# Performance work log

Hardware: AMD Instinct MI355X
Metric: run time of the kernel (lower is better)

## Reference

```python
import jax, jax.numpy as jnp
import numpy as np

B, T, E = 2, 2048, 2048
H, KV, D = 16, 4, 128
N_REP = H // KV
WINDOW = 512
BASE_THETA = 10000.0
MIN_VAL = -1e9


def _rope_cos_sin(seq_len, dim, dtype):
    inv_freq = 1.0 / (BASE_THETA ** (jnp.arange(0, dim, 2, dtype=jnp.float32) / dim))
    ang = jnp.arange(seq_len, dtype=jnp.float32)[:, None] * inv_freq[None, :]  # [T, D/2]
    return jnp.cos(ang).astype(dtype), jnp.sin(ang).astype(dtype)


def _apply_rope(x, cos, sin):
    # x: [B, T, h, D]; rotate-half convention
    x1, x2 = jnp.split(x, 2, axis=-1)
    c = cos[None, :, None, :]
    s = sin[None, :, None, :]
    return jnp.concatenate([x1 * c - x2 * s, x2 * c + x1 * s], axis=-1)


def setup_inputs() -> dict:
    key = jax.random.key(0)
    k1, k2, k3, k4, k5 = jax.random.split(key, 5)
    std = 0.02 / np.sqrt(2 * 24)
    return {
        "x": jax.random.normal(k1, (B, T, E), dtype=jnp.float32),
        "Wq": jax.random.normal(k2, (H * D, E), dtype=jnp.float32) * std,
        "Wk": jax.random.normal(k3, (KV * D, E), dtype=jnp.float32) * std,
        "Wv": jax.random.normal(k4, (KV * D, E), dtype=jnp.float32) * std,
        "Wo": jax.random.normal(k5, (E, E), dtype=jnp.float32) * std,
    }


def reference(x, Wq, Wk, Wv, Wo):
    b, t, e = x.shape
    scale = 1.0 / jnp.sqrt(jnp.float32(D))

    q = (x @ Wq.T).reshape(b, t, H, D)
    k = (x @ Wk.T).reshape(b, t, KV, D)
    v = (x @ Wv.T).reshape(b, t, KV, D)

    cos, sin = _rope_cos_sin(t, D, x.dtype)
    q = _apply_rope(q, cos, sin)
    k = _apply_rope(k, cos, sin)

    # GQA: repeat kv heads to match query heads
    k = jnp.repeat(k, N_REP, axis=2)  # [B, T, H, D]
    v = jnp.repeat(v, N_REP, axis=2)

    scores = jnp.einsum("bqhd,bkhd->bhqk", q, k) * scale  # [B, H, T, T]

    # sliding-window causal additive mask (offset=0)
    rows = jnp.arange(t)[:, None]
    cols = jnp.arange(t)[None, :]
    valid = (cols <= rows) & ((rows - cols) < WINDOW)
    mask = jnp.where(valid, 0.0, MIN_VAL).astype(x.dtype)  # [T, T]
    scores = scores + mask[None, None, :, :]

    attn = jax.nn.softmax(scores, axis=-1)
    out = jnp.einsum("bhqk,bkhd->bqhd", attn, v).reshape(b, t, H * D)
    return out @ Wo.T
```

## Files before the change

kernel.cpp:

```cpp
#include <hip/hip_runtime.h>
#include <hip/hip_bf16.h>
#include <cstdint>

#define TSEQ 2048
#define NB   2
#define NH   16
#define NKV  4
#define HD   128
#define EMB  2048
#define WIN  512

typedef unsigned short u16;
typedef __attribute__((ext_vector_type(8))) short s16x8;
typedef __attribute__((ext_vector_type(4))) float f32x4;
typedef __attribute__((ext_vector_type(16))) float f32x16;
typedef __attribute__((ext_vector_type(4))) unsigned short u16x4;
typedef __attribute__((ext_vector_type(8))) unsigned short u16x8;

__device__ __forceinline__ u16 f2bf(float x) {
    unsigned u = __builtin_bit_cast(unsigned, x);
    u += 0x7fffu + ((u >> 16) & 1u);
    return (u16)(u >> 16);
}
__device__ __forceinline__ float bf2f(u16 u) {
    return __builtin_bit_cast(float, ((unsigned)u) << 16);
}
__device__ __forceinline__ float ex2(float x) {
    return __builtin_amdgcn_exp2f(x);
}

__device__ __forceinline__ void gld_lds16(const void* g, void* l) {
    __builtin_amdgcn_global_load_lds(
        (__attribute__((address_space(1))) void*)(void*)(g),
        (__attribute__((address_space(3))) void*)(l),
        16, 0, 0);
}

__device__ __forceinline__ f32x4 mfma16(s16x8 a, s16x8 b, f32x4 c) {
    return __builtin_amdgcn_mfma_f32_16x16x32_bf16(a, b, c, 0, 0, 0);
}
__device__ __forceinline__ f32x16 mfma32(s16x8 a, s16x8 b, f32x16 c) {
    return __builtin_amdgcn_mfma_f32_32x32x16_bf16(a, b, c, 0, 0, 0);
}

template <int CTRL>
__device__ __forceinline__ float dpp_movf(float x) {
    return __builtin_bit_cast(float,
        __builtin_amdgcn_update_dpp(0, __builtin_bit_cast(int, x), CTRL, 0xF, 0xF, true));
}
__device__ __forceinline__ float dpp_max16(float x) {
    x = fmaxf(x, dpp_movf<0xB1>(x));
    x = fmaxf(x, dpp_movf<0x4E>(x));
    x = fmaxf(x, dpp_movf<0x128>(x));
    x = fmaxf(x, dpp_movf<0x124>(x));
    return x;
}
__device__ __forceinline__ float dpp_sum16(float x) {
    x += dpp_movf<0xB1>(x);
    x += dpp_movf<0x4E>(x);
    x += dpp_movf<0x128>(x);
    x += dpp_movf<0x124>(x);
    return x;
}

__global__ void cast_all(const float* __restrict__ x,  const float* __restrict__ wq,
                         const float* __restrict__ wk, const float* __restrict__ wv,
                         const float* __restrict__ wo,
                         u16* __restrict__ xb, u16* __restrict__ wqb,
                         u16* __restrict__ wkvb, u16* __restrict__ wob,
                         float* __restrict__ tab) {
    if (blockIdx.x >= 18432) {
        int i = (blockIdx.x - 18432) * 256 + threadIdx.x;
        int t = i >> 6, d = i & 63;
        float inv = __expf(-(float)d * (9.210340371976184f / 64.0f));
        float s, c;
        sincosf((float)t * inv, &s, &c);
        tab[i] = c;
        tab[131072 + i] = s;
        return;
    }
    long i = ((long)blockIdx.x * 256 + threadIdx.x) * 4;
    const float* s; u16* d; long off;
    if (i < 8388608L)        { s = x;  d = xb;             off = i; }
    else if (i < 12582912L)  { s = wq; d = wqb;            off = i - 8388608L; }
    else if (i < 13631488L)  { s = wk; d = wkvb;           off = i - 12582912L; }
    else if (i < 14680064L)  { s = wv; d = wkvb + 1048576; off = i - 13631488L; }
    else                     { s = wo; d = wob;            off = i - 14680064L; }
    float4 v = *(const float4*)(s + off);
    u16x4 o;
    o[0] = f2bf(v.x); o[1] = f2bf(v.y); o[2] = f2bf(v.z); o[3] = f2bf(v.w);
    *(u16x4*)(d + off) = o;
}

#define RDFRAG(base, offb, sg, ks) \
    (*(const s16x8*)((base) + (offb) + ((((half) + 2 * (ks)) ^ (sg)) << 4)))

template <int MODE>
__global__ __launch_bounds__(512) void gemm8(const u16* __restrict__ A, const u16* __restrict__ B,
                                             void* __restrict__ Cp, u16* __restrict__ vtp,
                                             u16* __restrict__ kp) {
    constexpr int BN     = (MODE == 3) ? 192 : 128;
    constexpr int NBB    = BN / 64;
    constexpr int K      = 2048;
    constexpr int NTK    = K / 64;
    constexpr int ABYTES = 32768;
    constexpr int BBYTES = BN * 128;
    constexpr int BUFB   = ABYTES + BBYTES;
    constexpr int NLD    = 4 + NBB;

    __shared__ __align__(16) char smem[2 * BUFB];

    const int tid  = threadIdx.x;
    const int lane = tid & 63;
    const int w    = tid >> 6;
    const int l31  = lane & 31;
    const int half = lane >> 5;
    const int wr   = w >> 1;
    const int wc   = w & 1;
    const int bx   = blockIdx.x, by = blockIdx.y;

    const int srow   = w * 8 + (lane >> 3);
    const int schunk = lane & 7;
    const int sdoff  = w * 8 * 128;

    const u16* agp[4];
    const u16* bgp[NBB];
#pragma unroll
    for (int s = 0; s < 4; s++) {
        const int row = s * 64 + srow;
        const int sg  = ((row >> 1) ^ (row >> 2)) & 7;
        agp[s] = A + (size_t)(by * 256 + row) * K + ((schunk ^ sg) << 3);
    }
#pragma unroll
    for (int s = 0; s < NBB; s++) {
        const int row = s * 64 + srow;
        const int sg  = ((row >> 1) ^ (row >> 2)) & 7;
        bgp[s] = B + (size_t)(bx * BN + row) * K + ((schunk ^ sg) << 3);
    }

    int aoffb[2], asg[2];
#pragma unroll
    for (int mi = 0; mi < 2; mi++) {
        const int r = wr * 64 + mi * 32 + l31;
        aoffb[mi] = r * 128;
        asg[mi]   = ((r >> 1) ^ (r >> 2)) & 7;
    }
    int boffb[NBB], bsg[NBB];
#pragma unroll
    for (int nj = 0; nj < NBB; nj++) {
        const int r = wc * (BN / 2) + nj * 32 + l31;
        boffb[nj] = r * 128;
        bsg[nj]   = ((r >> 1) ^ (r >> 2)) & 7;
    }

    f32x16 acc[2][NBB];
#pragma unroll
    for (int mi = 0; mi < 2; mi++)
#pragma unroll
        for (int nj = 0; nj < NBB; nj++)
#pragma unroll
            for (int r = 0; r < 16; r++)
                acc[mi][nj][r] = 0.f;

    auto stage_A = [&](char* base) {
#pragma unroll
        for (int s = 0; s < 4; s++) {
            gld_lds16(agp[s], base + s * 8192 + sdoff);
            agp[s] += 64;
        }
    };
    auto stage_B = [&](char* base) {
#pragma unroll
        for (int s = 0; s < NBB; s++) {
            gld_lds16(bgp[s], base + ABYTES + s * 8192 + sdoff);
            bgp[s] += 64;
        }
    };

    stage_A(smem);        stage_B(smem);
    stage_A(smem + BUFB); stage_B(smem + BUFB);

    for (int t = 0; t < NTK; ++t) {
        char* buf = smem + (t & 1) * BUFB;
        const char* Ab = buf;
        const char* Bb = buf + ABYTES;
        if (t < NTK - 1) asm volatile("s_waitcnt vmcnt(%0)" :: "n"(NLD) : "memory");
        else             asm volatile("s_waitcnt vmcnt(0)" ::: "memory");
        __builtin_amdgcn_s_barrier();

        s16x8 a0[4], a1[4];
        {
            s16x8 bf[4];
#pragma unroll
            for (int ks = 0; ks < 4; ks++) {
                a0[ks] = RDFRAG(Ab, aoffb[0], asg[0], ks);
                a1[ks] = RDFRAG(Ab, aoffb[1], asg[1], ks);
                bf[ks] = RDFRAG(Bb, boffb[0], bsg[0], ks);
            }
            __builtin_amdgcn_s_barrier();
            __builtin_amdgcn_s_setprio(1);
#pragma unroll
            for (int ks = 0; ks < 4; ks++) {
                acc[0][0] = mfma32(a0[ks], bf[ks], acc[0][0]);
                acc[1][0] = mfma32(a1[ks], bf[ks], acc[1][0]);
            }
            __builtin_amdgcn_s_setprio(0);
            __builtin_amdgcn_s_barrier();
        }
        asm volatile("" ::: "memory");
        if (t + 2 < NTK) stage_A(buf);
#pragma unroll
        for (int j = 1; j < NBB; j++) {
            s16x8 bf[4];
#pragma unroll
            for (int ks = 0; ks < 4; ks++)
                bf[ks] = RDFRAG(Bb, boffb[j], bsg[j], ks);
            __builtin_amdgcn_s_barrier();
            __builtin_amdgcn_s_setprio(1);
#pragma unroll
            for (int ks = 0; ks < 4; ks++) {
                acc[0][j] = mfma32(a0[ks], bf[ks], acc[0][j]);
                acc[1][j] = mfma32(a1[ks], bf[ks], acc[1][j]);
            }
            __builtin_amdgcn_s_setprio(0);
            __builtin_amdgcn_s_barrier();
        }
        asm volatile("" ::: "memory");
        if (t + 2 < NTK) stage_B(buf);
    }

    const int row0 = by * 256 + wr * 64;
    if constexpr (MODE == 0) {
        const int col0 = bx * 128 + wc * 64 + l31;
#pragma unroll
        for (int mi = 0; mi < 2; mi++)
#pragma unroll
            for (int nj = 0; nj < 2; nj++)
#pragma unroll
                for (int r = 0; r < 16; r++) {
                    const int crow = row0 + mi * 32 + (r & 3) + 8 * (r >> 2) + 4 * half;
                    ((float*)Cp)[(size_t)crow * 2048 + col0 + nj * 32] = acc[mi][nj][r];
                }
    } else {
#pragma unroll
        for (int nj = 0; nj < NBB; nj++) {
            const int colbase = bx * 192 + wc * 96 + nj * 32;
            if (colbase >= 2560) continue;
            if (colbase < 2048) {
#pragma unroll
                for (int mi = 0; mi < 2; mi++)
#pragma unroll
                    for (int r = 0; r < 16; r++) {
                        const int crow = row0 + mi * 32 + (r & 3) + 8 * (r >> 2) + 4 * half;
                        ((u16*)Cp)[(size_t)crow * 2048 + colbase + l31] = f2bf(acc[mi][nj][r]);
                    }
            } else {
#pragma unroll
                for (int mi = 0; mi < 2; mi++)
#pragma unroll
                    for (int r = 0; r < 16; r++) {
                        const int crow = row0 + mi * 32 + (r & 3) + 8 * (r >> 2) + 4 * half;
                        kp[(size_t)crow * 512 + colbase - 2048 + l31] = f2bf(acc[mi][nj][r]);
                    }
            }
        }
        const int bb = (by * 256) >> 11;
        const int t0 = (by * 256) & (TSEQ - 1);
        u16* tr = (u16*)smem;
#pragma unroll
        for (int wcx = 0; wcx < 2; wcx++)
#pragma unroll
            for (int njx = 0; njx < NBB; njx++) {
                const int colbase = bx * 192 + wcx * 96 + njx * 32;
                if (colbase < 2560) continue;
                __syncthreads();
                if (wc == wcx) {
#pragma unroll
                    for (int mi = 0; mi < 2; mi++)
#pragma unroll
                        for (int r = 0; r < 16; r++) {
                            const int tl = wr * 64 + mi * 32 + (r & 3) + 8 * (r >> 2) + 4 * half;
                            tr[l31 * 264 + tl] = f2bf(acc[mi][njx][r]);
                        }
                }
                __syncthreads();
                const int voff = colbase - 2560;
#pragma unroll
                for (int s = 0; s < 2; s++) {
                    const int slot = s * 512 + tid;
                    const int dl   = slot >> 5;
                    const int tseg = slot & 31;
                    u16x8 val = *(const u16x8*)(tr + dl * 264 + tseg * 8);
                    const int dg = voff + dl;
                    *(u16x8*)(vtp + ((size_t)((bb * NKV + (dg >> 7)) * HD + (dg & 127))) * TSEQ +
                              t0 + tseg * 8) = val;
                }
            }
    }
}

__global__ void rope_k(u16* __restrict__ buf, const float* __restrict__ tab) {
    int i = blockIdx.x * 256 + threadIdx.x;
    int d   = i & 63;
    int hh  = (i >> 6) & 3;
    int row = i >> 8;
    int t   = row & (TSEQ - 1);
    size_t base = (size_t)row * 512 + hh * HD + d;
    float x1 = bf2f(buf[base]);
    float x2 = bf2f(buf[base + 64]);
    float c = tab[t * 64 + d];
    float s = tab[131072 + t * 64 + d];
    buf[base]      = f2bf(x1 * c - x2 * s);
    buf[base + 64] = f2bf(x2 * c + x1 * s);
}

__global__ __launch_bounds__(256, 3) void attn_kernel(const u16* __restrict__ qb, const u16* __restrict__ kb,
                                                      const u16* __restrict__ vt, const float* __restrict__ tab,
                                                      u16* __restrict__ ao) {
    __shared__ __align__(16) char smem[40960];
    u16* ks = (u16*)smem;
    u16* vs = (u16*)(smem + 16384);
    u16* Pl = (u16*)(smem + 32768);

    const int tid  = threadIdx.x;
    const int w    = tid >> 6;
    const int lane = tid & 63;
    const int l15  = lane & 15;
    const int quad = lane >> 4;
    const int id   = blockIdx.x;
    const int kv   = id & 3;
    const int b    = (id >> 2) & 1;
    const int q0   = (id >> 3) * 16;
    const int h    = kv * 4 + w;
    u16* Pw = Pl + w * 1024;
    const float scale2 = 0.1275174089593282f;

    const u16* kbase = kb + (size_t)b * TSEQ * 512 + kv * HD;
    const u16* vbase = vt + (size_t)(b * NKV + kv) * HD * TSEQ;

    s16x8 aq[4];
    {
        const u16* qrow = qb + (size_t)(b * TSEQ + q0 + l15) * EMB + h * HD + quad * 8;
        const float* ct = tab + (size_t)(q0 + l15) * 64 + quad * 8;
        float qf[4][8], cs[2][8], sn[2][8];
        *(float4*)(&cs[0][0]) = *(const float4*)(ct);
        *(float4*)(&cs[0][4]) = *(const float4*)(ct + 4);
        *(float4*)(&cs[1][0]) = *(const float4*)(ct + 32);
        *(float4*)(&cs[1][4]) = *(const float4*)(ct + 36);
        *(float4*)(&sn[0][0]) = *(const float4*)(ct + 131072);
        *(float4*)(&sn[0][4]) = *(const float4*)(ct + 131076);
        *(float4*)(&sn[1][0]) = *(const float4*)(ct + 131104);
        *(float4*)(&sn[1][4]) = *(const float4*)(ct + 131108);
#pragma unroll
        for (int c = 0; c < 4; c++)
#pragma unroll
            for (int e = 0; e < 8; e++)
                qf[c][e] = bf2f(qrow[c * 32 + e]);
#pragma unroll
        for (int c = 0; c < 2; c++)
#pragma unroll
            for (int e = 0; e < 8; e++) {
                float x1 = qf[c][e], x2 = qf[c + 2][e];
                qf[c][e]     = x1 * cs[c][e] - x2 * sn[c][e];
                qf[c + 2][e] = x2 * cs[c][e] + x1 * sn[c][e];
            }
#pragma unroll
        for (int c = 0; c < 4; c++)
#pragma unroll
            for (int e = 0; e < 8; e++)
                aq[c][e] = (short)f2bf(qf[c][e]);
    }

    f32x4 o[8];
#pragma unroll
    for (int n = 0; n < 8; n++) o[n] = f32x4{0.f, 0.f, 0.f, 0.f};
    float mrow[4] = {-1e30f, -1e30f, -1e30f, -1e30f};
    float lrow[4] = {0.f, 0.f, 0.f, 0.f};

    int kb0 = q0 - (WIN - 1);
    if (kb0 < 0) kb0 = 0;
    kb0 &= ~63;

    for (int kbi = kb0; kbi <= q0 + 15; kbi += 64) {
#pragma unroll
        for (int s = 0; s < 4; s++) {
            int slot = s * 256 + tid;
            int i    = slot >> 4;
            int lc   = (slot & 15) ^ (i & 7);
            gld_lds16(kbase + (size_t)(kbi + i) * 512 + lc * 8, (char*)ks + slot * 16);
        }
#pragma unroll
        for (int s = 0; s < 4; s++) {
            int slot = s * 256 + tid;
            int d    = slot >> 3;
            int lc   = (slot & 7) ^ (d & 7);
            gld_lds16(vbase + (size_t)d * TSEQ + kbi + lc * 8, (char*)vs + slot * 16);
        }
        __syncthreads();

        f32x4 sv[4];
#pragma unroll
        for (int kt = 0; kt < 4; kt++) sv[kt] = f32x4{0.f, 0.f, 0.f, 0.f};
#pragma unroll
        for (int c = 0; c < 4; c++) {
            s16x8 bk[4];
#pragma unroll
            for (int kt = 0; kt < 4; kt++) {
                int sc = (c * 4 + quad) ^ (l15 & 7);
                bk[kt] = *(const s16x8*)(ks + (kt * 16 + l15) * 128 + sc * 8);
            }
#pragma unroll
            for (int kt = 0; kt < 4; kt++)
                sv[kt] = mfma16(aq[c], bk[kt], sv[kt]);
        }

        const bool full = (kbi >= q0 - 496) && (kbi + 63 <= q0);
        float alpha[4], p[4][4];
#pragma unroll
        for (int r = 0; r < 4; r++) {
            const int row = q0 + quad * 4 + r;
            float v[4];
            if (full) {
#pragma unroll
                for (int kt = 0; kt < 4; kt++) v[kt] = sv[kt][r] * scale2;
            } else {
#pragma unroll
                for (int kt = 0; kt < 4; kt++) {
                    int cidx = kbi + kt * 16 + l15;
                    v[kt] = (cidx <= row && row - cidx < WIN) ? sv[kt][r] * scale2 : -1e30f;
                }
            }
            float mx = fmaxf(fmaxf(v[0], v[1]), fmaxf(v[2], v[3]));
            mx = dpp_max16(mx);
            float mnew = fmaxf(mrow[r], mx);
            alpha[r] = ex2(mrow[r] - mnew);
            float e0 = ex2(v[0] - mnew);
            float e1 = ex2(v[1] - mnew);
            float e2 = ex2(v[2] - mnew);
            float e3 = ex2(v[3] - mnew);
            float rs = (e0 + e1) + (e2 + e3);
            rs = dpp_sum16(rs);
            lrow[r] = lrow[r] * alpha[r] + rs;
            mrow[r] = mnew;
            p[0][r] = e0; p[1][r] = e1; p[2][r] = e2; p[3][r] = e3;
        }
#pragma unroll
        for (int n = 0; n < 8; n++) {
            o[n][0] *= alpha[0]; o[n][1] *= alpha[1];
            o[n][2] *= alpha[2]; o[n][3] *= alpha[3];
        }

#pragma unroll
        for (int r = 0; r < 4; r++)
#pragma unroll
            for (int kt = 0; kt < 4; kt++)
                Pw[(kt >> 1) * 512 + (quad * 4 + r) * 32 + (kt & 1) * 16 + l15] = f2bf(p[kt][r]);
        asm volatile("s_waitcnt lgkmcnt(0)" ::: "memory");
        s16x8 ap0 = *(const s16x8*)(Pw + l15 * 32 + quad * 8);
        s16x8 ap1 = *(const s16x8*)(Pw + 512 + l15 * 32 + quad * 8);

#pragma unroll
        for (int n = 0; n < 8; n++) {
            int sc = quad ^ (l15 & 7);
            s16x8 bv = *(const s16x8*)(vs + (n * 16 + l15) * 64 + sc * 8);
            o[n] = mfma16(ap0, bv, o[n]);
        }
#pragma unroll
        for (int n = 0; n < 8; n++) {
            int sc = (4 + quad) ^ (l15 & 7);
            s16x8 bv = *(const s16x8*)(vs + (n * 16 + l15) * 64 + sc * 8);
            o[n] = mfma16(ap1, bv, o[n]);
        }
        __syncthreads();
    }

    float linv[4];
#pragma unroll
    for (int r = 0; r < 4; r++) linv[r] = 1.0f / lrow[r];
    u16* Ow = (u16*)(smem + w * 4352);
#pragma unroll
    for (int n = 0; n < 8; n++)
#pragma unroll
        for (int r = 0; r < 4; r++)
            Ow[(quad * 4 + r) * 136 + n * 16 + l15] = f2bf(o[n][r] * linv[r]);
    asm volatile("s_waitcnt lgkmcnt(0)" ::: "memory");
#pragma unroll
    for (int s = 0; s < 4; s++) {
        int row = s * 4 + quad;
        u16x8 val = *(const u16x8*)(Ow + row * 136 + l15 * 8);
        *(u16x8*)(ao + (size_t)(b * TSEQ + q0 + row) * EMB + h * HD + l15 * 8) = val;
    }
}

extern "C" void kernel_launch(void* const* d_in, const int* in_sizes, int n_in,
                              void* d_out, int out_size, void* d_ws, size_t ws_size,
                              hipStream_t stream) {
    const float* x  = (const float*)d_in[0];
    const float* Wq = (const float*)d_in[1];
    const float* Wk = (const float*)d_in[2];
    const float* Wv = (const float*)d_in[3];
    const float* Wo = (const float*)d_in[4];
    float* out = (float*)d_out;

    u16* ws   = (u16*)d_ws;
    u16* xb   = ws;
    u16* wqb  = ws + 8388608L;
    u16* wkvb = ws + 12582912L;
    u16* wob  = ws + 14680064L;
    u16* qb   = ws + 18874368L;
    u16* kbuf = ws + 27262976L;
    u16* vt   = ws + 29360128L;
    float* tab = (float*)(ws + 31457280L);
    u16* ao   = xb;

    cast_all<<<18944, 256, 0, stream>>>(x, Wq, Wk, Wv, Wo, xb, wqb, wkvb, wob, tab);

    gemm8<3><<<dim3(16, 16), 512, 0, stream>>>(xb, wqb, qb, vt, kbuf);

    rope_k<<<4096, 256, 0, stream>>>(kbuf, tab);

    attn_kernel<<<1024, 256, 0, stream>>>(qb, kbuf, vt, tab, ao);

    gemm8<0><<<dim3(16, 16), 512, 0, stream>>>(ao, wob, out, nullptr, nullptr);
}
```

Before: 253.2 us.

## Restructure GEMM main loop into two k-phases with merged A/B staging

The GEMM inner loop used to read A fragments once, then walk the B column blocks one at a time, issuing the A prefetch partway through and the B prefetch at the end. It now splits each k-tile into two phases that each read all A and B fragments for half the k-steps, wait on LDS, then issue every MFMA. A and B global-to-LDS staging is merged into a single call after both phases. This cuts barriers per tile and gives larger MFMA bursts, but the next tile's loads are issued later and more fragment registers stay live at once.

```diff
diff --git a/kernel.cpp b/kernel.cpp
--- a/kernel.cpp
+++ b/kernel.cpp
@@ -162,14 +162,12 @@
             for (int r = 0; r < 16; r++)
                 acc[mi][nj][r] = 0.f;
 
-    auto stage_A = [&](char* base) {
+    auto stage_AB = [&](char* base) {
 #pragma unroll
         for (int s = 0; s < 4; s++) {
             gld_lds16(agp[s], base + s * 8192 + sdoff);
             agp[s] += 64;
         }
-    };
-    auto stage_B = [&](char* base) {
 #pragma unroll
         for (int s = 0; s < NBB; s++) {
             gld_lds16(bgp[s], base + ABYTES + s * 8192 + sdoff);
@@ -177,8 +175,8 @@
         }
     };
 
-    stage_A(smem);        stage_B(smem);
-    stage_A(smem + BUFB); stage_B(smem + BUFB);
+    stage_AB(smem);
+    stage_AB(smem + BUFB);
 
     for (int t = 0; t < NTK; ++t) {
         char* buf = smem + (t & 1) * BUFB;
@@ -188,45 +186,37 @@
         else             asm volatile("s_waitcnt vmcnt(0)" ::: "memory");
         __builtin_amdgcn_s_barrier();
 
-        s16x8 a0[4], a1[4];
-        {
-            s16x8 bf[4];
-#pragma unroll
-            for (int ks = 0; ks < 4; ks++) {
-                a0[ks] = RDFRAG(Ab, aoffb[0], asg[0], ks);
-                a1[ks] = RDFRAG(Ab, aoffb[1], asg[1], ks);
-                bf[ks] = RDFRAG(Bb, boffb[0], bsg[0], ks);
+#pragma unroll
+        for (int ph = 0; ph < 2; ph++) {
+            s16x8 af[2][2], bf[NBB][2];
+#pragma unroll
+            for (int ks2 = 0; ks2 < 2; ks2++) {
+                const int ks = ph * 2 + ks2;
+#pragma unroll
+                for (int mi = 0; mi < 2; mi++)
+                    af[mi][ks2] = RDFRAG(Ab, aoffb[mi], asg[mi], ks);
+#pragma unroll
+                for (int nj = 0; nj < NBB; nj++)
+                    bf[nj][ks2] = RDFRAG(Bb, boffb[nj], bsg[nj], ks);
             }
+            __builtin_amdgcn_sched_barrier(0);
             __builtin_amdgcn_s_barrier();
+            asm volatile("s_waitcnt lgkmcnt(0)" ::: "memory");
+            __builtin_amdgcn_sched_barrier(0);
             __builtin_amdgcn_s_setprio(1);
 #pragma unroll
-            for (int ks = 0; ks < 4; ks++) {
-                acc[0][0] = mfma32(a0[ks], bf[ks], acc[0][0]);
-                acc[1][0] = mfma32(a1[ks], bf[ks], acc[1][0]);
-            }
+            for (int ks2 = 0; ks2 < 2; ks2++)
+#pragma unroll
+                for (int mi = 0; mi < 2; mi++)
+#pragma unroll
+                    for (int nj = 0; nj < NBB; nj++)
+                        acc[mi][nj] = mfma32(af[mi][ks2], bf[nj][ks2], acc[mi][nj]);
             __builtin_amdgcn_s_setprio(0);
+            __builtin_amdgcn_sched_barrier(0);
             __builtin_amdgcn_s_barrier();
         }
         asm volatile("" ::: "memory");
-        if (t + 2 < NTK) stage_A(buf);
-#pragma unroll
-        for (int j = 1; j < NBB; j++) {
-            s16x8 bf[4];
-#pragma unroll
-            for (int ks = 0; ks < 4; ks++)
-                bf[ks] = RDFRAG(Bb, boffb[j], bsg[j], ks);
-            __builtin_amdgcn_s_barrier();
-            __builtin_amdgcn_s_setprio(1);
-#pragma unroll
-            for (int ks = 0; ks < 4; ks++) {
-                acc[0][j] = mfma32(a0[ks], bf[ks], acc[0][j]);
-                acc[1][j] = mfma32(a1[ks], bf[ks], acc[1][j]);
-            }
-            __builtin_amdgcn_s_setprio(0);
-            __builtin_amdgcn_s_barrier();
-        }
-        asm volatile("" ::: "memory");
-        if (t + 2 < NTK) stage_B(buf);
+        if (t + 2 < NTK) stage_AB(buf);
     }
 
     const int row0 = by * 256 + wr * 64;
```

After: 257.0 us. About the same (+1.5%).
